# Kernel optimization log

Measured on AMD Instinct MI355X. Metric: run time of the kernel, lower is better.

## Reference

```python
import jax, jax.numpy as jnp
import numpy as np

VOCAB, E, H, OUT = 128, 768, 768, 768
B, T = 128, 512


def setup_inputs() -> dict:
    key = jax.random.key(0)
    ks = jax.random.split(key, 8)
    s_emb = 1.0  # torch nn.Embedding default init is N(0,1)
    s_gru = 1.0 / np.sqrt(H)  # torch GRU init U(-1/sqrt(H), 1/sqrt(H))
    s_fc = 1.0 / np.sqrt(H)
    return {
        "x": jax.random.randint(ks[0], (B, T), 0, VOCAB),
        "emb": jax.random.normal(ks[1], (VOCAB, E), dtype=jnp.float32) * s_emb,
        "W_ih": jax.random.uniform(ks[2], (3 * H, E), jnp.float32, -s_gru, s_gru),
        "W_hh": jax.random.uniform(ks[3], (3 * H, H), jnp.float32, -s_gru, s_gru),
        "b_ih": jax.random.uniform(ks[4], (3 * H,), jnp.float32, -s_gru, s_gru),
        "b_hh": jax.random.uniform(ks[5], (3 * H,), jnp.float32, -s_gru, s_gru),
        "fc_W": jax.random.uniform(ks[6], (OUT, H), jnp.float32, -s_fc, s_fc),
        "fc_b": jax.random.uniform(ks[7], (OUT,), jnp.float32, -s_fc, s_fc),
    }


def _gru_last_hidden(xe, W_ih, W_hh, b_ih, b_hh):
    # xe: [B, T, E]. Precompute all input-side gate pre-activations in one GEMM.
    gx = jnp.einsum("bte,ge->btg", xe, W_ih) + b_ih  # [B, T, 3H]
    gx = jnp.swapaxes(gx, 0, 1)  # [T, B, 3H] for scan
    h0 = jnp.zeros((xe.shape[0], W_hh.shape[1]), xe.dtype)

    def step(h, gx_t):
        gh = h @ W_hh.T + b_hh  # [B, 3H]
        xr, xz, xn = jnp.split(gx_t, 3, axis=-1)
        hr, hz, hn = jnp.split(gh, 3, axis=-1)
        r = jax.nn.sigmoid(xr + hr)
        z = jax.nn.sigmoid(xz + hz)
        n = jnp.tanh(xn + r * hn)
        h_new = (1.0 - z) * n + z * h
        return h_new, None

    h_last, _ = jax.lax.scan(step, h0, gx)
    return h_last  # [B, H]


def reference(x, emb, W_ih, W_hh, b_ih, b_hh, fc_W, fc_b):
    xe = jnp.take(emb, x, axis=0)  # [B, T, E]
    h = _gru_last_hidden(xe, W_ih, W_hh, b_ih, b_hh)
    return h @ fc_W.T + fc_b  # [B, OUT]
```

## Files before the change

### kernel.cpp

```cpp
#include <hip/hip_runtime.h>

#define DI __device__ __forceinline__

constexpr int BB   = 128;
constexpr int TT   = 512;
constexpr int HH   = 768;
constexpr int G3   = 3 * HH;
constexpr int VOC  = 128;

constexpr int NG   = 8;
constexpr int NW   = 48;
constexpr int KC   = 24;
constexpr int FPAD = 16;

constexpr size_t OFF_GE   = 0;
constexpr size_t OFF_WIMG = 1179648;
constexpr size_t OFF_H16  = OFF_WIMG + 3538944;
constexpr size_t OFF_H32  = OFF_H16 + 393216;
constexpr size_t OFF_FLG  = OFF_H32 + 393216;

constexpr int LDS_W_BYTES = 3 * KC * 64 * 16;
constexpr int LDS_BYTES   = LDS_W_BYTES + 1024;

typedef _Float16 f16x8 __attribute__((ext_vector_type(8)));
typedef float    f32x4 __attribute__((ext_vector_type(4)));

DI float sigm(float x) { return __builtin_amdgcn_rcpf(1.0f + __expf(-x)); }
DI float tanh_fast(float x) {
  float e = __expf(-2.0f * fabsf(x));
  float r = (1.0f - e) * __builtin_amdgcn_rcpf(1.0f + e);
  return copysignf(r, x);
}

DI f16x8 load_dc_x4(const void* p) {
  f16x8 r;
  asm volatile("global_load_dwordx4 %0, %1, off sc1"
               : "=v"(r) : "v"(p) : "memory");
  return r;
}
DI void store_dc_x2(void* p, uint2 v) {
  asm volatile("global_store_dwordx2 %0, %1, off sc1"
               :: "v"(p), "v"(v) : "memory");
}
DI int load_flag(const int* p) {
  int r;
  asm volatile("global_load_dword %0, %1, off sc1\n\ts_waitcnt vmcnt(0)"
               : "=v"(r) : "v"(p) : "memory");
  return r;
}
DI void store_flag(int* p, int v) {
  asm volatile("global_store_dword %0, %1, off sc1"
               :: "v"(p), "v"(v) : "memory");
}
DI void wait_vm0() { asm volatile("s_waitcnt vmcnt(0)" ::: "memory"); }
DI void wait_lgkm0() { asm volatile("s_waitcnt lgkmcnt(0)" ::: "memory"); }

__global__ void k_zero(int* flg, int n) {
  int i = blockIdx.x * 256 + threadIdx.x;
  if (i < n) flg[i] = 0;
}

__global__ void k_prep_w(const float* __restrict__ Whh, _Float16* __restrict__ wimg) {
  int tid = blockIdx.x * 256 + threadIdx.x;
  if (tid >= NW * 3 * KC * 64) return;
  int l  = tid & 63;
  int fi = tid >> 6;
  int kc = fi % KC;
  int nt = (fi / KC) % 3;
  int j  = fi / (KC * 3);
  int g  = nt * HH + j * 16 + (l & 15);
  int k0 = kc * 32 + (l >> 4) * 8;
  const float* src = Whh + (size_t)g * HH + k0;
  f16x8 o;
#pragma unroll
  for (int q = 0; q < 8; ++q) o[q] = (_Float16)src[q];
  ((f16x8*)wimg)[tid] = o;
}

__global__ void k_prep_ge(const float* __restrict__ emb, const float* __restrict__ Wih,
                          const float* __restrict__ bih, float* __restrict__ ge) {
  int g  = blockIdx.x * 256 + threadIdx.x;
  int v0 = blockIdx.y * 16;
  float acc[16];
  float b = bih[g];
#pragma unroll
  for (int i = 0; i < 16; ++i) acc[i] = b;
  const float* wrow = Wih + (size_t)g * HH;
  for (int e = 0; e < HH; e += 4) {
    float4 w = *(const float4*)(wrow + e);
#pragma unroll
    for (int i = 0; i < 16; ++i) {
      float4 m = *(const float4*)(emb + (size_t)(v0 + i) * HH + e);
      acc[i] = fmaf(w.x, m.x, acc[i]);
      acc[i] = fmaf(w.y, m.y, acc[i]);
      acc[i] = fmaf(w.z, m.z, acc[i]);
      acc[i] = fmaf(w.w, m.w, acc[i]);
    }
  }
#pragma unroll
  for (int i = 0; i < 16; ++i) ge[(size_t)(v0 + i) * G3 + g] = acc[i];
}

__global__ __launch_bounds__(64, 1) void k_gru(
    const int* __restrict__ x,
    const float* __restrict__ ge,
    const float* __restrict__ bhh,
    const _Float16* __restrict__ wimg,
    _Float16* h16,
    float* __restrict__ h32,
    int* flg)
{
  extern __shared__ char smem[];
  _Float16* st = (_Float16*)(smem + LDS_W_BYTES);

  const int lane = threadIdx.x;
  const int bid  = blockIdx.x;
  const int grp  = bid / NW;
  const int j    = bid % NW;
  const int bm   = grp * 16;
  const int u0   = j * 16;
  int* gflg = flg + grp * NW * FPAD;

  {
    const uint4* src = (const uint4*)(wimg + (size_t)j * (3 * KC * 64 * 8));
    uint4* dst = (uint4*)smem;
#pragma unroll 8
    for (int r = 0; r < 72; ++r) dst[lane + 64 * r] = src[lane + 64 * r];
  }

  const int c16 = lane & 15;
  const int kr  = lane >> 4;

  const float bh_r = bhh[0 * HH + u0 + c16];
  const float bh_z = bhh[1 * HH + u0 + c16];
  const float bh_n = bhh[2 * HH + u0 + c16];

  float hprev[4] = {0.f, 0.f, 0.f, 0.f};

  _Float16* hb0 = h16;
  _Float16* hb1 = h16 + (size_t)BB * HH;
  const f16x8* bfr = (const f16x8*)smem;

  const int fidx = (lane < NW) ? lane : (lane - NW);
  const int* fpoll = gflg + fidx * FPAD;

  float ger[4], gez[4], gen[4];
#pragma unroll
  for (int q = 0; q < 4; ++q) {
    int xv = x[(size_t)(bm + kr * 4 + q) * TT + 0];
    const float* gp = ge + (size_t)xv * G3 + u0 + c16;
    ger[q] = gp[0 * HH];
    gez[q] = gp[1 * HH];
    gen[q] = gp[2 * HH];
  }

  int budget = 1 << 20;

  for (int t = 0; t < TT; ++t) {
    int xvn[4];
    if (t < TT - 1) {
#pragma unroll
      for (int q = 0; q < 4; ++q)
        xvn[q] = x[(size_t)(bm + kr * 4 + q) * TT + (t + 1)];
    }

    f32x4 acc0 = {bh_r, bh_r, bh_r, bh_r};
    f32x4 acc1 = {bh_z, bh_z, bh_z, bh_z};
    f32x4 acc2 = {bh_n, bh_n, bh_n, bh_n};

    if (t > 0) {
      for (;;) {
        int f = load_flag(fpoll);
        if (__all(f >= t)) break;
        if (--budget < 0) break;
      }
      asm volatile("" ::: "memory");

      const _Float16* hb = (t & 1) ? hb1 : hb0;
      const char* ab = (const char*)(hb + (size_t)(bm + c16) * HH) + kr * 16;
      f16x8 a[KC];
#pragma unroll
      for (int kc = 0; kc < KC; ++kc) a[kc] = load_dc_x4(ab + kc * 64);
      wait_vm0();
      __builtin_amdgcn_sched_barrier(0);

#pragma unroll
      for (int kc = 0; kc < KC; ++kc) {
        acc0 = __builtin_amdgcn_mfma_f32_16x16x32_f16(a[kc], bfr[(0 * KC + kc) * 64 + lane], acc0, 0, 0, 0);
        acc1 = __builtin_amdgcn_mfma_f32_16x16x32_f16(a[kc], bfr[(1 * KC + kc) * 64 + lane], acc1, 0, 0, 0);
        acc2 = __builtin_amdgcn_mfma_f32_16x16x32_f16(a[kc], bfr[(2 * KC + kc) * 64 + lane], acc2, 0, 0, 0);
      }
    }

    float hv[4];
#pragma unroll
    for (int q = 0; q < 4; ++q) {
      float r = sigm(acc0[q] + ger[q]);
      float z = sigm(acc1[q] + gez[q]);
      float n = tanh_fast(gen[q] + r * acc2[q]);
      float h = n + z * (hprev[q] - n);
      hprev[q] = h;
      hv[q] = h;
    }

    if (t == TT - 1) {
#pragma unroll
      for (int q = 0; q < 4; ++q)
        h32[(size_t)(bm + kr * 4 + q) * HH + u0 + c16] = hv[q];
    } else {
#pragma unroll
      for (int q = 0; q < 4; ++q)
        st[(kr * 4 + q) * 20 + c16] = (_Float16)hv[q];

#pragma unroll
      for (int q = 0; q < 4; ++q) {
        const float* gp = ge + (size_t)xvn[q] * G3 + u0 + c16;
        ger[q] = gp[0 * HH];
        gez[q] = gp[1 * HH];
        gen[q] = gp[2 * HH];
      }

      wait_lgkm0();
      __builtin_amdgcn_sched_barrier(0);
      int rr = lane >> 2;
      int qq = lane & 3;
      uint2 v = *(const uint2*)&st[rr * 20 + qq * 4];
      _Float16* hn = (t & 1) ? hb0 : hb1;
      store_dc_x2((char*)(hn + (size_t)(bm + rr) * HH + u0 + qq * 4), v);

      wait_vm0();
      if (lane == 0) store_flag(gflg + j * FPAD, t + 1);
    }
  }
}

__global__ void k_fc(const float* __restrict__ h32, const float* __restrict__ fcW,
                     const float* __restrict__ fcb, float* __restrict__ out) {
  int o  = blockIdx.x * 256 + threadIdx.x;
  int b0 = blockIdx.y * 16;
  float acc[16];
  float bi = fcb[o];
#pragma unroll
  for (int i = 0; i < 16; ++i) acc[i] = bi;
  const float* wrow = fcW + (size_t)o * HH;
  for (int e = 0; e < HH; e += 4) {
    float4 w = *(const float4*)(wrow + e);
#pragma unroll
    for (int i = 0; i < 16; ++i) {
      float4 m = *(const float4*)(h32 + (size_t)(b0 + i) * HH + e);
      acc[i] = fmaf(w.x, m.x, acc[i]);
      acc[i] = fmaf(w.y, m.y, acc[i]);
      acc[i] = fmaf(w.z, m.z, acc[i]);
      acc[i] = fmaf(w.w, m.w, acc[i]);
    }
  }
#pragma unroll
  for (int i = 0; i < 16; ++i) out[(size_t)(b0 + i) * HH + o] = acc[i];
}

extern "C" void kernel_launch(void* const* d_in, const int* in_sizes, int n_in,
                              void* d_out, int out_size, void* d_ws, size_t ws_size,
                              hipStream_t stream) {
  const int*   x   = (const int*)d_in[0];
  const float* emb = (const float*)d_in[1];
  const float* Wih = (const float*)d_in[2];
  const float* Whh = (const float*)d_in[3];
  const float* bih = (const float*)d_in[4];
  const float* bhh = (const float*)d_in[5];
  const float* fcW = (const float*)d_in[6];
  const float* fcb = (const float*)d_in[7];
  float* out = (float*)d_out;

  char* ws = (char*)d_ws;
  float*     ge   = (float*)(ws + OFF_GE);
  _Float16*  wimg = (_Float16*)(ws + OFF_WIMG);
  _Float16*  h16  = (_Float16*)(ws + OFF_H16);
  float*     h32  = (float*)(ws + OFF_H32);
  int*       flg  = (int*)(ws + OFF_FLG);

  k_zero<<<24, 256, 0, stream>>>(flg, NG * NW * FPAD);
  k_prep_w<<<864, 256, 0, stream>>>(Whh, wimg);
  k_prep_ge<<<dim3(9, 8), 256, 0, stream>>>(emb, Wih, bih, ge);

  hipFuncSetAttribute(reinterpret_cast<const void*>(k_gru),
                      hipFuncAttributeMaxDynamicSharedMemorySize, LDS_BYTES);
  k_gru<<<NG * NW, 64, LDS_BYTES, stream>>>(x, ge, bhh, wimg, h16, h32, flg);

  k_fc<<<dim3(3, 8), 256, 0, stream>>>(h32, fcW, fcb, out);
}
```

Before: 2.314 ms.

## Pack two GRU wavefronts per block, pipeline flag polling, defer gate loads

Each workgroup now holds two independent 64-lane waves, each owning its own column tile and its own LDS weight slice. This halves the block count to 192 while keeping the same 384-wave persistent layout. The flag spin-wait swaps the blocking load-plus-waitcnt for six in-flight relaxed agent-scope atomic loads, which cuts the time between a producer's flag store and its detection. The next step's input-gate gathers move after the flag store, so publishing h is not delayed by those loads. The risks are LDS pressure from doubled weight storage per block and more cache traffic from the extra polling loads.

```diff
diff --git a/kernel.cpp b/kernel.cpp
--- a/kernel.cpp
+++ b/kernel.cpp
@@ -20,7 +20,7 @@
 constexpr size_t OFF_FLG  = OFF_H32 + 393216;
 
 constexpr int LDS_W_BYTES = 3 * KC * 64 * 16;
-constexpr int LDS_BYTES   = LDS_W_BYTES + 1024;
+constexpr int LDS_BYTES   = 2 * LDS_W_BYTES + 2048;
 
 typedef _Float16 f16x8 __attribute__((ext_vector_type(8)));
 typedef float    f32x4 __attribute__((ext_vector_type(4)));
@@ -42,18 +42,14 @@
   asm volatile("global_store_dwordx2 %0, %1, off sc1"
                :: "v"(p), "v"(v) : "memory");
 }
-DI int load_flag(const int* p) {
-  int r;
-  asm volatile("global_load_dword %0, %1, off sc1\n\ts_waitcnt vmcnt(0)"
-               : "=v"(r) : "v"(p) : "memory");
-  return r;
-}
 DI void store_flag(int* p, int v) {
   asm volatile("global_store_dword %0, %1, off sc1"
                :: "v"(p), "v"(v) : "memory");
 }
 DI void wait_vm0() { asm volatile("s_waitcnt vmcnt(0)" ::: "memory"); }
 DI void wait_lgkm0() { asm volatile("s_waitcnt lgkmcnt(0)" ::: "memory"); }
+
+#define LDF(p) __hip_atomic_load((p), __ATOMIC_RELAXED, __HIP_MEMORY_SCOPE_AGENT)
 
 __global__ void k_zero(int* flg, int n) {
   int i = blockIdx.x * 256 + threadIdx.x;
@@ -101,7 +97,7 @@
   for (int i = 0; i < 16; ++i) ge[(size_t)(v0 + i) * G3 + g] = acc[i];
 }
 
-__global__ __launch_bounds__(64, 1) void k_gru(
+__global__ __launch_bounds__(128, 1) void k_gru(
     const int* __restrict__ x,
     const float* __restrict__ ge,
     const float* __restrict__ bhh,
@@ -111,19 +107,23 @@
     int* flg)
 {
   extern __shared__ char smem[];
-  _Float16* st = (_Float16*)(smem + LDS_W_BYTES);
-
-  const int lane = threadIdx.x;
+
+  const int tid  = threadIdx.x;
+  const int lane = tid & 63;
+  const int wid  = tid >> 6;
   const int bid  = blockIdx.x;
-  const int grp  = bid / NW;
-  const int j    = bid % NW;
+  const int grp  = bid / 24;
+  const int j    = 2 * (bid % 24) + wid;
   const int bm   = grp * 16;
   const int u0   = j * 16;
   int* gflg = flg + grp * NW * FPAD;
 
+  char* mysmem = smem + wid * LDS_W_BYTES;
+  _Float16* st = (_Float16*)(smem + 2 * LDS_W_BYTES) + wid * 320;
+
   {
     const uint4* src = (const uint4*)(wimg + (size_t)j * (3 * KC * 64 * 8));
-    uint4* dst = (uint4*)smem;
+    uint4* dst = (uint4*)mysmem;
 #pragma unroll 8
     for (int r = 0; r < 72; ++r) dst[lane + 64 * r] = src[lane + 64 * r];
   }
@@ -139,7 +139,7 @@
 
   _Float16* hb0 = h16;
   _Float16* hb1 = h16 + (size_t)BB * HH;
-  const f16x8* bfr = (const f16x8*)smem;
+  const f16x8* bfr = (const f16x8*)mysmem;
 
   const int fidx = (lane < NW) ? lane : (lane - NW);
   const int* fpoll = gflg + fidx * FPAD;
@@ -154,7 +154,7 @@
     gen[q] = gp[2 * HH];
   }
 
-  int budget = 1 << 20;
+  int budget = 1 << 21;
 
   for (int t = 0; t < TT; ++t) {
     int xvn[4];
@@ -169,10 +169,18 @@
     f32x4 acc2 = {bh_n, bh_n, bh_n, bh_n};
 
     if (t > 0) {
-      for (;;) {
-        int f = load_flag(fpoll);
-        if (__all(f >= t)) break;
-        if (--budget < 0) break;
+      {
+        int f0 = LDF(fpoll), f1 = LDF(fpoll), f2 = LDF(fpoll),
+            f3 = LDF(fpoll), f4 = LDF(fpoll), f5 = LDF(fpoll);
+        for (;;) {
+          if (__all(f0 >= t)) break; f0 = LDF(fpoll);
+          if (__all(f1 >= t)) break; f1 = LDF(fpoll);
+          if (__all(f2 >= t)) break; f2 = LDF(fpoll);
+          if (__all(f3 >= t)) break; f3 = LDF(fpoll);
+          if (__all(f4 >= t)) break; f4 = LDF(fpoll);
+          if (__all(f5 >= t)) break; f5 = LDF(fpoll);
+          if ((budget -= 6) < 0) break;
+        }
       }
       asm volatile("" ::: "memory");
 
@@ -211,15 +219,6 @@
 #pragma unroll
       for (int q = 0; q < 4; ++q)
         st[(kr * 4 + q) * 20 + c16] = (_Float16)hv[q];
-
-#pragma unroll
-      for (int q = 0; q < 4; ++q) {
-        const float* gp = ge + (size_t)xvn[q] * G3 + u0 + c16;
-        ger[q] = gp[0 * HH];
-        gez[q] = gp[1 * HH];
-        gen[q] = gp[2 * HH];
-      }
-
       wait_lgkm0();
       __builtin_amdgcn_sched_barrier(0);
       int rr = lane >> 2;
@@ -230,6 +229,14 @@
 
       wait_vm0();
       if (lane == 0) store_flag(gflg + j * FPAD, t + 1);
+
+#pragma unroll
+      for (int q = 0; q < 4; ++q) {
+        const float* gp = ge + (size_t)xvn[q] * G3 + u0 + c16;
+        ger[q] = gp[0 * HH];
+        gez[q] = gp[1 * HH];
+        gen[q] = gp[2 * HH];
+      }
     }
   }
 }
@@ -284,7 +291,7 @@
 
   hipFuncSetAttribute(reinterpret_cast<const void*>(k_gru),
                       hipFuncAttributeMaxDynamicSharedMemorySize, LDS_BYTES);
-  k_gru<<<NG * NW, 64, LDS_BYTES, stream>>>(x, ge, bhh, wimg, h16, h32, flg);
+  k_gru<<<192, 128, LDS_BYTES, stream>>>(x, ge, bhh, wimg, h16, h32, flg);
 
   k_fc<<<dim3(3, 8), 256, 0, stream>>>(h32, fcW, fcb, out);
 }
```

Result: slower. 2.557 ms (+10.5%).

## Replace flag-after-store handshake with poisoned 8-slot hidden-state ring

Applied to the files above, without the earlier changes.

The hidden-state exchange moves from a double buffer into an 8-slot per-group ring whose slots are pre-filled with fp16 infinity. The producer no longer waits for its h store to complete (wait_vm0) before raising the flag. Consumers instead re-read the data until no poison pattern remains, and producers re-poison a slot ahead of reuse. The aim is to take the store-completion wait off the per-step critical path. In exchange it adds a validation loop and an extra poison store per step, and it is wrong if a legitimate hidden value is ever inf or NaN.

```diff
diff --git a/kernel.cpp b/kernel.cpp
--- a/kernel.cpp
+++ b/kernel.cpp
@@ -13,10 +13,14 @@
 constexpr int KC   = 24;
 constexpr int FPAD = 16;
 
+constexpr int ROWB = HH * 2;
+constexpr int SLOT = 16 * ROWB;
+constexpr size_t GR_RING = (size_t)8 * SLOT;
+
 constexpr size_t OFF_GE   = 0;
 constexpr size_t OFF_WIMG = 1179648;
-constexpr size_t OFF_H16  = OFF_WIMG + 3538944;
-constexpr size_t OFF_H32  = OFF_H16 + 393216;
+constexpr size_t OFF_RING = OFF_WIMG + 3538944;
+constexpr size_t OFF_H32  = OFF_RING + NG * GR_RING;
 constexpr size_t OFF_FLG  = OFF_H32 + 393216;
 
 constexpr int LDS_W_BYTES = 3 * KC * 64 * 16;
@@ -24,6 +28,7 @@
 
 typedef _Float16 f16x8 __attribute__((ext_vector_type(8)));
 typedef float    f32x4 __attribute__((ext_vector_type(4)));
+typedef unsigned int u32x4 __attribute__((ext_vector_type(4)));
 
 DI float sigm(float x) { return __builtin_amdgcn_rcpf(1.0f + __expf(-x)); }
 DI float tanh_fast(float x) {
@@ -58,6 +63,11 @@
 __global__ void k_zero(int* flg, int n) {
   int i = blockIdx.x * 256 + threadIdx.x;
   if (i < n) flg[i] = 0;
+}
+__global__ void k_poison(u32x4* ring, int n16) {
+  int i = blockIdx.x * 256 + threadIdx.x;
+  u32x4 p = {0x7C007C00u, 0x7C007C00u, 0x7C007C00u, 0x7C007C00u};
+  if (i < n16) ring[i] = p;
 }
 
 __global__ void k_prep_w(const float* __restrict__ Whh, _Float16* __restrict__ wimg) {
@@ -106,7 +116,7 @@
     const float* __restrict__ ge,
     const float* __restrict__ bhh,
     const _Float16* __restrict__ wimg,
-    _Float16* h16,
+    char* ring,
     float* __restrict__ h32,
     int* flg)
 {
@@ -119,6 +129,7 @@
   const int j    = bid % NW;
   const int bm   = grp * 16;
   const int u0   = j * 16;
+  char* gring = ring + (size_t)grp * GR_RING;
   int* gflg = flg + grp * NW * FPAD;
 
   {
@@ -136,10 +147,12 @@
   const float bh_n = bhh[2 * HH + u0 + c16];
 
   float hprev[4] = {0.f, 0.f, 0.f, 0.f};
-
-  _Float16* hb0 = h16;
-  _Float16* hb1 = h16 + (size_t)BB * HH;
   const f16x8* bfr = (const f16x8*)smem;
+
+  const int rr = lane >> 2;
+  const int qq = lane & 3;
+  const size_t pub_off = (size_t)rr * ROWB + (u0 + qq * 4) * 2;
+  const size_t con_off = (size_t)c16 * ROWB + kr * 16;
 
   const int fidx = (lane < NW) ? lane : (lane - NW);
   const int* fpoll = gflg + fidx * FPAD;
@@ -176,12 +189,33 @@
       }
       asm volatile("" ::: "memory");
 
-      const _Float16* hb = (t & 1) ? hb1 : hb0;
-      const char* ab = (const char*)(hb + (size_t)(bm + c16) * HH) + kr * 16;
+      const char* ab = gring + (size_t)(t & 7) * SLOT + con_off;
       f16x8 a[KC];
 #pragma unroll
       for (int kc = 0; kc < KC; ++kc) a[kc] = load_dc_x4(ab + kc * 64);
       wait_vm0();
+      __builtin_amdgcn_sched_barrier(0);
+      {
+        unsigned bad = 0;
+#pragma unroll
+        for (int kc = 0; kc < KC; ++kc) {
+          u32x4 u = *(const u32x4*)&a[kc];
+          bad |= ((u.x & 0x7C00u) == 0x7C00u) | ((u.z & 0x7C00u) == 0x7C00u);
+        }
+        while (__any(bad)) {
+          if (--budget < 0) break;
+#pragma unroll
+          for (int kc = 0; kc < KC; ++kc) a[kc] = load_dc_x4(ab + kc * 64);
+          wait_vm0();
+          __builtin_amdgcn_sched_barrier(0);
+          bad = 0;
+#pragma unroll
+          for (int kc = 0; kc < KC; ++kc) {
+            u32x4 u = *(const u32x4*)&a[kc];
+            bad |= ((u.x & 0x7C00u) == 0x7C00u) | ((u.z & 0x7C00u) == 0x7C00u);
+          }
+        }
+      }
       __builtin_amdgcn_sched_barrier(0);
 
 #pragma unroll
@@ -211,6 +245,14 @@
 #pragma unroll
       for (int q = 0; q < 4; ++q)
         st[(kr * 4 + q) * 20 + c16] = (_Float16)hv[q];
+      wait_lgkm0();
+      __builtin_amdgcn_sched_barrier(0);
+      uint2 v = *(const uint2*)&st[rr * 20 + qq * 4];
+
+      store_dc_x2(gring + (size_t)((t + 1) & 7) * SLOT + pub_off, v);
+      uint2 pz; pz.x = 0x7C007C00u; pz.y = 0x7C007C00u;
+      store_dc_x2(gring + (size_t)((t + 6) & 7) * SLOT + pub_off, pz);
+      if (lane == 0) store_flag(gflg + j * FPAD, t + 1);
 
 #pragma unroll
       for (int q = 0; q < 4; ++q) {
@@ -219,17 +261,6 @@
         gez[q] = gp[1 * HH];
         gen[q] = gp[2 * HH];
       }
-
-      wait_lgkm0();
-      __builtin_amdgcn_sched_barrier(0);
-      int rr = lane >> 2;
-      int qq = lane & 3;
-      uint2 v = *(const uint2*)&st[rr * 20 + qq * 4];
-      _Float16* hn = (t & 1) ? hb0 : hb1;
-      store_dc_x2((char*)(hn + (size_t)(bm + rr) * HH + u0 + qq * 4), v);
-
-      wait_vm0();
-      if (lane == 0) store_flag(gflg + j * FPAD, t + 1);
     }
   }
 }
@@ -274,17 +305,18 @@
   char* ws = (char*)d_ws;
   float*     ge   = (float*)(ws + OFF_GE);
   _Float16*  wimg = (_Float16*)(ws + OFF_WIMG);
-  _Float16*  h16  = (_Float16*)(ws + OFF_H16);
+  char*      ring = ws + OFF_RING;
   float*     h32  = (float*)(ws + OFF_H32);
   int*       flg  = (int*)(ws + OFF_FLG);
 
   k_zero<<<24, 256, 0, stream>>>(flg, NG * NW * FPAD);
+  k_poison<<<384, 256, 0, stream>>>((u32x4*)ring, 98304);
   k_prep_w<<<864, 256, 0, stream>>>(Whh, wimg);
   k_prep_ge<<<dim3(9, 8), 256, 0, stream>>>(emb, Wih, bih, ge);
 
   hipFuncSetAttribute(reinterpret_cast<const void*>(k_gru),
                       hipFuncAttributeMaxDynamicSharedMemorySize, LDS_BYTES);
-  k_gru<<<NG * NW, 64, LDS_BYTES, stream>>>(x, ge, bhh, wimg, h16, h32, flg);
+  k_gru<<<NG * NW, 64, LDS_BYTES, stream>>>(x, ge, bhh, wimg, ring, h32, flg);
 
   k_fc<<<dim3(3, 8), 256, 0, stream>>>(h32, fcW, fcb, out);
 }
```

Measured after the change: 2.385 ms. +3.1%, slower.
